# Kernel tuning notes

Hardware: AMD Instinct MI355X
Metric: run time of the kernel (lower is better)

The kernel has to match this reference:

```python
import jax, jax.numpy as jnp
from jax import lax
import numpy as np

H = 64  # hidden size

def lstm_layer(x, w_ih, w_hh, b_ih, b_hh):
    # x: [B,T,I]; w_ih: [4H,I]; w_hh: [4H,H]; gates ordered i,f,g,o (PyTorch)
    B = x.shape[0]
    xg = jnp.einsum('bti,gi->btg', x, w_ih) + b_ih  # precompute input projections [B,T,4H]
    h0 = jnp.zeros((B, H), x.dtype)
    c0 = jnp.zeros((B, H), x.dtype)
    def step(carry, xt):
        h, c = carry
        gates = xt + h @ w_hh.T + b_hh
        i, f, g, o = jnp.split(gates, 4, axis=-1)
        c = jax.nn.sigmoid(f) * c + jax.nn.sigmoid(i) * jnp.tanh(g)
        h = jax.nn.sigmoid(o) * jnp.tanh(c)
        return (h, c), h
    (hT, cT), hs = lax.scan(step, (h0, c0), jnp.swapaxes(xg, 0, 1))
    return jnp.swapaxes(hs, 0, 1), hT, cT

def layernorm(x, g, b, eps=1e-5):
    mu = jnp.mean(x, axis=-1, keepdims=True)
    var = jnp.mean(jnp.square(x - mu), axis=-1, keepdims=True)
    return (x - mu) * lax.rsqrt(var + eps) * g + b

def setup_inputs() -> dict:
    key = jax.random.key(0)
    ks = jax.random.split(key, 16)
    s = 0.05
    return {
        'x': jax.random.normal(ks[0], (512, 1024, 32), jnp.float32),
        'w_ih1': jax.random.normal(ks[1], (4 * H, 32)) * s,
        'w_hh1': jax.random.normal(ks[2], (4 * H, H)) * s,
        'b_ih1': jax.random.normal(ks[3], (4 * H,)) * s,
        'b_hh1': jax.random.normal(ks[4], (4 * H,)) * s,
        'w_ih2': jax.random.normal(ks[5], (4 * H, H)) * s,
        'w_hh2': jax.random.normal(ks[6], (4 * H, H)) * s,
        'b_ih2': jax.random.normal(ks[7], (4 * H,)) * s,
        'b_hh2': jax.random.normal(ks[8], (4 * H,)) * s,
        'fc1_w': jax.random.normal(ks[9], (128, H)) * s,
        'fc1_b': jax.random.normal(ks[10], (128,)) * s,
        'fc2_w': jax.random.normal(ks[11], (128, 128)) * s,
        'fc2_b': jax.random.normal(ks[12], (128,)) * s,
        'ln_g': jnp.ones((128,), jnp.float32),
        'ln_b': jnp.zeros((128,), jnp.float32),
    }

def reference(x, w_ih1, w_hh1, b_ih1, b_hh1, w_ih2, w_hh2, b_ih2, b_hh2,
              fc1_w, fc1_b, fc2_w, fc2_b, ln_g, ln_b):
    h1, _, _ = lstm_layer(x, w_ih1, w_hh1, b_ih1, b_hh1)
    # dropout(0.1) is identity in eval mode
    _, hT, _ = lstm_layer(h1, w_ih2, w_hh2, b_ih2, b_hh2)
    y = jax.nn.relu(hT @ fc1_w.T + fc1_b)
    y = y @ fc2_w.T + fc2_b
    return layernorm(y, ln_g, ln_b)
```

## Files before the change

### kernel.cpp

```cpp
#include <hip/hip_runtime.h>
#include <cstdint>
#include <cstddef>

#define T_STEPS 1024
#define NBLK    256
#define LOG2E   1.4426950408889634f

typedef __attribute__((ext_vector_type(8))) _Float16 half8;
typedef __attribute__((ext_vector_type(4))) _Float16 half4;
typedef __attribute__((ext_vector_type(4))) float    f32x4;
typedef __attribute__((ext_vector_type(4))) int      i32x4;

static __device__ __forceinline__ float fexp2(float x) {
#if defined(__has_builtin) && __has_builtin(__builtin_amdgcn_exp2f)
  return __builtin_amdgcn_exp2f(x);
#else
  return __exp2f(x);
#endif
}
static __device__ __forceinline__ float sigm2(float a) {
  return __builtin_amdgcn_rcpf(1.0f + fexp2(-a));
}
static __device__ __forceinline__ float tanhg2(float a) {
  return 2.0f * __builtin_amdgcn_rcpf(1.0f + fexp2(-(a + a))) - 1.0f;
}
static __device__ __forceinline__ float tanhc(float c) {
  return 1.0f - 2.0f * __builtin_amdgcn_rcpf(1.0f + fexp2(c * (2.0f * LOG2E)));
}

static __device__ __forceinline__ half8 load8s(const float* s, float sc) {
  float4 a = ((const float4*)s)[0];
  float4 b = ((const float4*)s)[1];
  half8 h;
  h[0] = (_Float16)(a.x * sc); h[1] = (_Float16)(a.y * sc);
  h[2] = (_Float16)(a.z * sc); h[3] = (_Float16)(a.w * sc);
  h[4] = (_Float16)(b.x * sc); h[5] = (_Float16)(b.y * sc);
  h[6] = (_Float16)(b.z * sc); h[7] = (_Float16)(b.w * sc);
  return h;
}
static __device__ __forceinline__ half4 cvt4(float4 v) {
  half4 h; h[0] = (_Float16)v.x; h[1] = (_Float16)v.y; h[2] = (_Float16)v.z; h[3] = (_Float16)v.w;
  return h;
}
static __device__ __forceinline__ i32x4 quant16(const float* src, float s) {
  union { i32x4 v; signed char b[16]; } u;
  #pragma unroll
  for (int j = 0; j < 16; ++j) u.b[j] = (signed char)__float2int_rn(src[j] * s);
  return u.v;
}

static __device__ __forceinline__ void barrier_lds() {
  __asm__ volatile("s_waitcnt lgkmcnt(0)\n\ts_barrier" ::: "memory");
}

__global__ __launch_bounds__(512, 2) void lstm_fused(
    const float* __restrict__ x,
    const float* __restrict__ w_ih1, const float* __restrict__ w_hh1,
    const float* __restrict__ b_ih1, const float* __restrict__ b_hh1,
    const float* __restrict__ w_ih2, const float* __restrict__ w_hh2,
    const float* __restrict__ b_ih2, const float* __restrict__ b_hh2,
    const float* __restrict__ fc1_w, const float* __restrict__ fc1_b,
    const float* __restrict__ fc2_w, const float* __restrict__ fc2_b,
    const float* __restrict__ ln_g, const float* __restrict__ ln_b,
    float* __restrict__ out)
{
  __shared__ __align__(16) signed char hs8[2][2][2][64];
  __shared__ __align__(16) _Float16 xbig[2][16][2][32];
  __shared__ __align__(16) float hfin[2][64];
  __shared__ __align__(16) float y1s[2][128];
  __shared__ __align__(16) float y2s[2][128];
  __shared__ float redmu[2], redrs[2];

  const int t   = threadIdx.x;
  const int b   = blockIdx.x;
  const int l   = t & 63;
  const int w   = t >> 6;
  const int ly  = w >> 2;
  const int wq  = w & 3;
  const int col = l & 15;
  const int q   = l >> 4;
  const int bm  = ((l & 15) >> 2) & 1;

  if (t < 512) ((signed char*)hs8)[t] = 0;

  if (t < 256) {
    const int b0 = t >> 7, r0 = t & 127, tr0 = r0 >> 3, ii0 = r0 & 7;
    const float4 v = *(const float4*)(x + ((size_t)(2 * b + b0) * T_STEPS + tr0) * 32 + ii0 * 4);
    *(half4*)((char*)xbig + tr0 * 128 + b0 * 64 + ii0 * 8) = cvt4(v);
  }

  half8 wbx[4];
  i32x4 wqa[4], wqb[4];
  float fs[4];
  {
    #pragma unroll
    for (int tt = 0; tt < 4; ++tt) {
      const int r = tt * 64 + wq * 16 + col;
      if (ly == 0) {
        wbx[tt] = load8s(w_ih1 + r * 32 + q * 8, LOG2E);
        const float* s1 = w_hh1 + r * 64 + q * 16;
        float m = 0.0f;
        #pragma unroll
        for (int j = 0; j < 16; ++j) m = fmaxf(m, fabsf(s1[j]));
        m = fmaxf(m, __shfl_xor(m, 16, 64));
        m = fmaxf(m, __shfl_xor(m, 32, 64));
        const float s = 127.0f / m;
        wqa[tt] = quant16(s1, s);
        wqb[tt] = wqa[tt];
        fs[tt] = m * (LOG2E / 16129.0f);
      } else {
        const float* s1 = w_ih2 + r * 64 + q * 16;
        const float* s2 = w_hh2 + r * 64 + q * 16;
        float m = 0.0f;
        #pragma unroll
        for (int j = 0; j < 16; ++j) m = fmaxf(m, fmaxf(fabsf(s1[j]), fabsf(s2[j])));
        m = fmaxf(m, __shfl_xor(m, 16, 64));
        m = fmaxf(m, __shfl_xor(m, 32, 64));
        const float s = 127.0f / m;
        wqa[tt] = quant16(s1, s);
        wqb[tt] = quant16(s2, s);
        fs[tt] = m * (LOG2E / 16129.0f);
      }
    }
  }

  float bia[4];
  f32x4 biav[4];
  {
    const float* bi_ = ly ? b_ih2 : b_ih1;
    const float* bh_ = ly ? b_hh2 : b_hh1;
    #pragma unroll
    for (int tt = 0; tt < 4; ++tt) {
      const int r = tt * 64 + wq * 16 + col;
      bia[tt] = (bi_[r] + bh_[r]) * LOG2E;
      biav[tt] = (f32x4){bia[tt], bia[tt], bia[tt], bia[tt]};
    }
  }
  const int u   = wq * 16 + col;
  const int abm = l >> 4;
  const int hwofs = ly * 128 + abm * 64 + u;

  const bool isx = (w < 4) && (l >= 32);
  const int g   = w * 32 + (l - 32);
  const int xtr = g >> 3;
  const int xii = g & 7;
  const float* xsrc0 = x + ((size_t)(2 * b + 0) * T_STEPS) * 32 + xii * 4;
  const float* xsrc1 = x + ((size_t)(2 * b + 1) * T_STEPS) * 32 + xii * 4;

  const char* h8base = (const char*)hs8  + bm * 64 + q * 16;
  const char* xwbase = (const char*)xbig + bm * 64 + q * 16;

  __syncthreads();

  half8 xf;
  i32x4 h1f;
  if (ly == 0) xf = *(const half8*)xwbase;

  float4 xv0 = make_float4(0.f, 0.f, 0.f, 0.f);
  float4 xv1 = make_float4(0.f, 0.f, 0.f, 0.f);
  float c = 0.0f;
  const i32x4 zi = (i32x4){0, 0, 0, 0};

  auto phase = [&](int p, int RD8, int WR8) {
    if (isx && (p & 15) == 0 && (p + 16 + xtr) < T_STEPS) {
      xv0 = *(const float4*)(xsrc0 + (size_t)(p + 16 + xtr) * 32);
      xv1 = *(const float4*)(xsrc1 + (size_t)(p + 16 + xtr) * 32);
    }

    if (ly == 0) {
      if (p < T_STEPS) {
        f32x4 accf[4];
        #pragma unroll
        for (int tt = 0; tt < 4; ++tt)
          accf[tt] = __builtin_amdgcn_mfma_f32_16x16x32_f16(xf, wbx[tt], biav[tt], 0, 0, 0);
        const i32x4 a1 = *(const i32x4*)(h8base + RD8);
        if (p + 1 < T_STEPS) {
          const int pn = p + 1;
          xf = *(const half8*)(xwbase + ((pn >> 4) & 1) * 2048 + (pn & 15) * 128);
        }
        i32x4 acci[4];
        #pragma unroll
        for (int tt = 0; tt < 4; ++tt)
          acci[tt] = __builtin_amdgcn_mfma_i32_16x16x64_i8(a1, wqa[tt], zi, 0, 0, 0);
        if (l < 32) {
          const float gi = sigm2 (accf[0][0] + fs[0] * (float)acci[0][0]);
          const float gf = sigm2 (accf[1][0] + fs[1] * (float)acci[1][0]);
          const float gg = tanhg2(accf[2][0] + fs[2] * (float)acci[2][0]);
          const float go = sigm2 (accf[3][0] + fs[3] * (float)acci[3][0]);
          c = gf * c + gi * gg;
          const float hv = go * tanhc(c);
          ((signed char*)hs8)[WR8 + hwofs] = (signed char)__float2int_rn(hv * 127.0f);
        }
      }
      if (isx && (p & 15) == 8 && (p + 8 + xtr) < T_STEPS) {
        const int bb2 = (((p >> 4) + 1) & 1) * 2048 + xtr * 128 + xii * 8;
        *(half4*)((char*)xbig + bb2)      = cvt4(xv0);
        *(half4*)((char*)xbig + bb2 + 64) = cvt4(xv1);
      }
    } else {
      i32x4 accq[4];
      if (p >= 2 && p <= T_STEPS + 1) {
        #pragma unroll
        for (int tt = 0; tt < 4; ++tt)
          accq[tt] = __builtin_amdgcn_mfma_i32_16x16x64_i8(h1f, wqa[tt], zi, 0, 0, 0);
      }
      i32x4 a2;
      if (p >= 2 && p <= T_STEPS + 1)
        a2 = *(const i32x4*)(h8base + RD8 + 128);
      if (p >= 1 && p <= T_STEPS)
        h1f = *(const i32x4*)(h8base + RD8);
      if (p >= 2 && p <= T_STEPS + 1) {
        i32x4 acci[4];
        #pragma unroll
        for (int tt = 0; tt < 4; ++tt)
          acci[tt] = __builtin_amdgcn_mfma_i32_16x16x64_i8(a2, wqb[tt], accq[tt], 0, 0, 0);
        if (l < 32) {
          const float gi = sigm2 (bia[0] + fs[0] * (float)acci[0][0]);
          const float gf = sigm2 (bia[1] + fs[1] * (float)acci[1][0]);
          const float gg = tanhg2(bia[2] + fs[2] * (float)acci[2][0]);
          const float go = sigm2 (bia[3] + fs[3] * (float)acci[3][0]);
          c = gf * c + gi * gg;
          const float hv = go * tanhc(c);
          ((signed char*)hs8)[WR8 + hwofs] = (signed char)__float2int_rn(hv * 127.0f);
          if (p == T_STEPS + 1) hfin[abm][u] = hv;
        }
      }
    }
  };

  for (int p2 = 0; p2 <= T_STEPS; p2 += 2) {
    phase(p2, 256, 0);
    barrier_lds();
    phase(p2 + 1, 0, 256);
    barrier_lds();
  }

  __syncthreads();

  if (t < 256) {
    const int bi = t >> 7, j = t & 127;
    float a = fc1_b[j];
    const float4* w4 = (const float4*)(fc1_w + j * 64);
    const float4* h4 = (const float4*)hfin[bi];
    #pragma unroll
    for (int qq = 0; qq < 16; ++qq) {
      float4 wv = w4[qq]; float4 hv = h4[qq];
      a += wv.x * hv.x + wv.y * hv.y + wv.z * hv.z + wv.w * hv.w;
    }
    y1s[bi][j] = fmaxf(a, 0.0f);
  }
  __syncthreads();
  if (t < 256) {
    const int bi = t >> 7, j = t & 127;
    float a = fc2_b[j];
    const float4* w4 = (const float4*)(fc2_w + j * 128);
    const float4* y4 = (const float4*)y1s[bi];
    #pragma unroll
    for (int qq = 0; qq < 32; ++qq) {
      float4 wv = w4[qq]; float4 yv = y4[qq];
      a += wv.x * yv.x + wv.y * yv.y + wv.z * yv.z + wv.w * yv.w;
    }
    y2s[bi][j] = a;
  }
  __syncthreads();
  if (t < 128) {
    const int bi = t >> 6, jj = t & 63;
    float s  = y2s[bi][jj] + y2s[bi][64 + jj];
    float qs = y2s[bi][jj] * y2s[bi][jj] + y2s[bi][64 + jj] * y2s[bi][64 + jj];
    #pragma unroll
    for (int off = 32; off > 0; off >>= 1) {
      s  += __shfl_down(s, off, 64);
      qs += __shfl_down(qs, off, 64);
    }
    if (jj == 0) {
      const float mu  = s * (1.0f / 128.0f);
      const float var = qs * (1.0f / 128.0f) - mu * mu;
      redmu[bi] = mu;
      redrs[bi] = rsqrtf(var + 1e-5f);
    }
  }
  __syncthreads();
  if (t < 256) {
    const int bi = t >> 7, j = t & 127;
    out[(size_t)(2 * b + bi) * 128 + j] =
        (y2s[bi][j] - redmu[bi]) * redrs[bi] * ln_g[j] + ln_b[j];
  }
}

extern "C" void kernel_launch(void* const* d_in, const int* in_sizes, int n_in,
                              void* d_out, int out_size, void* d_ws, size_t ws_size,
                              hipStream_t stream) {
  const float* x     = (const float*)d_in[0];
  const float* w_ih1 = (const float*)d_in[1];
  const float* w_hh1 = (const float*)d_in[2];
  const float* b_ih1 = (const float*)d_in[3];
  const float* b_hh1 = (const float*)d_in[4];
  const float* w_ih2 = (const float*)d_in[5];
  const float* w_hh2 = (const float*)d_in[6];
  const float* b_ih2 = (const float*)d_in[7];
  const float* b_hh2 = (const float*)d_in[8];
  const float* fc1_w = (const float*)d_in[9];
  const float* fc1_b = (const float*)d_in[10];
  const float* fc2_w = (const float*)d_in[11];
  const float* fc2_b = (const float*)d_in[12];
  const float* ln_g  = (const float*)d_in[13];
  const float* ln_b  = (const float*)d_in[14];
  float* out = (float*)d_out;

  lstm_fused<<<NBLK, 512, 0, stream>>>(x, w_ih1, w_hh1, b_ih1, b_hh1,
                                       w_ih2, w_hh2, b_ih2, b_hh2,
                                       fc1_w, fc1_b, fc2_w, fc2_b,
                                       ln_g, ln_b, out);
}
```

Before: 462.9 us.

## Restructure LSTM into warp-specialized segment pipeline with precomputed gate projections

```diff
diff --git a/kernel.cpp b/kernel.cpp
--- a/kernel.cpp
+++ b/kernel.cpp
@@ -3,11 +3,13 @@
 #include <cstddef>
 
 #define T_STEPS 1024
+#define SEG     8
+#define NSEG    (T_STEPS / SEG)
 #define NBLK    256
 #define LOG2E   1.4426950408889634f
+#define UPERM(k, c) ((((c) << 1) + ((k) & 1)) + (((k) >> 1) << 5))
 
 typedef __attribute__((ext_vector_type(8))) _Float16 half8;
-typedef __attribute__((ext_vector_type(4))) _Float16 half4;
 typedef __attribute__((ext_vector_type(4))) float    f32x4;
 typedef __attribute__((ext_vector_type(4))) int      i32x4;
 
@@ -38,10 +40,6 @@
   h[6] = (_Float16)(b.z * sc); h[7] = (_Float16)(b.w * sc);
   return h;
 }
-static __device__ __forceinline__ half4 cvt4(float4 v) {
-  half4 h; h[0] = (_Float16)v.x; h[1] = (_Float16)v.y; h[2] = (_Float16)v.z; h[3] = (_Float16)v.w;
-  return h;
-}
 static __device__ __forceinline__ i32x4 quant16(const float* src, float s) {
   union { i32x4 v; signed char b[16]; } u;
   #pragma unroll
@@ -53,7 +51,7 @@
   __asm__ volatile("s_waitcnt lgkmcnt(0)\n\ts_barrier" ::: "memory");
 }
 
-__global__ __launch_bounds__(512, 2) void lstm_fused(
+__global__ __launch_bounds__(256, 1) void lstm_fused(
     const float* __restrict__ x,
     const float* __restrict__ w_ih1, const float* __restrict__ w_hh1,
     const float* __restrict__ b_ih1, const float* __restrict__ b_hh1,
@@ -64,174 +62,214 @@
     const float* __restrict__ ln_g, const float* __restrict__ ln_b,
     float* __restrict__ out)
 {
-  __shared__ __align__(16) signed char hs8[2][2][2][64];
-  __shared__ __align__(16) _Float16 xbig[2][16][2][32];
+  __shared__ __align__(16) signed char h1ring[32][2][64];
+  __shared__ __align__(16) signed char h2ring[2][2][64];
+  __shared__ __align__(16) float xg1b[2][SEG][2][64][4];
+  __shared__ __align__(16) float xg2b[2][SEG][2][64][4];
   __shared__ __align__(16) float hfin[2][64];
   __shared__ __align__(16) float y1s[2][128];
   __shared__ __align__(16) float y2s[2][128];
   __shared__ float redmu[2], redrs[2];
 
   const int t   = threadIdx.x;
-  const int b   = blockIdx.x;
+  const int blk = blockIdx.x;
   const int l   = t & 63;
   const int w   = t >> 6;
-  const int ly  = w >> 2;
-  const int wq  = w & 3;
   const int col = l & 15;
   const int q   = l >> 4;
-  const int bm  = ((l & 15) >> 2) & 1;
-
-  if (t < 512) ((signed char*)hs8)[t] = 0;
-
-  if (t < 256) {
-    const int b0 = t >> 7, r0 = t & 127, tr0 = r0 >> 3, ii0 = r0 & 7;
-    const float4 v = *(const float4*)(x + ((size_t)(2 * b + b0) * T_STEPS + tr0) * 32 + ii0 * 4);
-    *(half4*)((char*)xbig + tr0 * 128 + b0 * 64 + ii0 * 8) = cvt4(v);
-  }
-
-  half8 wbx[4];
-  i32x4 wqa[4], wqb[4];
-  float fs[4];
+
   {
-    #pragma unroll
-    for (int tt = 0; tt < 4; ++tt) {
-      const int r = tt * 64 + wq * 16 + col;
-      if (ly == 0) {
-        wbx[tt] = load8s(w_ih1 + r * 32 + q * 8, LOG2E);
-        const float* s1 = w_hh1 + r * 64 + q * 16;
+    int* hp = (int*)h1ring;
+    #pragma unroll
+    for (int i = 0; i < 4; ++i) hp[t + i * 256] = 0;
+    if (t < 64) ((int*)h2ring)[t] = 0;
+  }
+
+  const i32x4 zi = (i32x4){0, 0, 0, 0};
+  f32x4 zf; zf[0] = 0.f; zf[1] = 0.f; zf[2] = 0.f; zf[3] = 0.f;
+
+  i32x4 wq[4][4];
+  half8 wbx[4][4];
+  f32x4 fsa0, fsa1;
+  float fsx[4][4];
+  float bL[4][4];
+
+  if (w < 3) {
+    const float* W = (w == 0) ? w_hh1 : (w == 1) ? w_hh2 : w_ih2;
+    float fs[4][4];
+    #pragma unroll
+    for (int g = 0; g < 4; ++g) {
+      #pragma unroll
+      for (int k = 0; k < 4; ++k) {
+        const int r = g * 64 + UPERM(k, col);
+        const float* p = W + r * 64 + q * 16;
         float m = 0.0f;
         #pragma unroll
-        for (int j = 0; j < 16; ++j) m = fmaxf(m, fabsf(s1[j]));
+        for (int j = 0; j < 16; ++j) m = fmaxf(m, fabsf(p[j]));
         m = fmaxf(m, __shfl_xor(m, 16, 64));
         m = fmaxf(m, __shfl_xor(m, 32, 64));
-        const float s = 127.0f / m;
-        wqa[tt] = quant16(s1, s);
-        wqb[tt] = wqa[tt];
-        fs[tt] = m * (LOG2E / 16129.0f);
-      } else {
-        const float* s1 = w_ih2 + r * 64 + q * 16;
-        const float* s2 = w_hh2 + r * 64 + q * 16;
-        float m = 0.0f;
+        wq[g][k] = quant16(p, 127.0f / m);
+        fs[g][k] = m * (LOG2E / 16129.0f);
+      }
+    }
+    if (w == 2) {
+      #pragma unroll
+      for (int g = 0; g < 4; ++g) {
         #pragma unroll
-        for (int j = 0; j < 16; ++j) m = fmaxf(m, fmaxf(fabsf(s1[j]), fabsf(s2[j])));
-        m = fmaxf(m, __shfl_xor(m, 16, 64));
-        m = fmaxf(m, __shfl_xor(m, 32, 64));
-        const float s = 127.0f / m;
-        wqa[tt] = quant16(s1, s);
-        wqb[tt] = quant16(s2, s);
-        fs[tt] = m * (LOG2E / 16129.0f);
-      }
-    }
-  }
-
-  float bia[4];
-  f32x4 biav[4];
-  {
-    const float* bi_ = ly ? b_ih2 : b_ih1;
-    const float* bh_ = ly ? b_hh2 : b_hh1;
-    #pragma unroll
-    for (int tt = 0; tt < 4; ++tt) {
-      const int r = tt * 64 + wq * 16 + col;
-      bia[tt] = (bi_[r] + bh_[r]) * LOG2E;
-      biav[tt] = (f32x4){bia[tt], bia[tt], bia[tt], bia[tt]};
-    }
-  }
-  const int u   = wq * 16 + col;
-  const int abm = l >> 4;
-  const int hwofs = ly * 128 + abm * 64 + u;
-
-  const bool isx = (w < 4) && (l >= 32);
-  const int g   = w * 32 + (l - 32);
-  const int xtr = g >> 3;
-  const int xii = g & 7;
-  const float* xsrc0 = x + ((size_t)(2 * b + 0) * T_STEPS) * 32 + xii * 4;
-  const float* xsrc1 = x + ((size_t)(2 * b + 1) * T_STEPS) * 32 + xii * 4;
-
-  const char* h8base = (const char*)hs8  + bm * 64 + q * 16;
-  const char* xwbase = (const char*)xbig + bm * 64 + q * 16;
-
-  __syncthreads();
-
-  half8 xf;
-  i32x4 h1f;
-  if (ly == 0) xf = *(const half8*)xwbase;
-
-  float4 xv0 = make_float4(0.f, 0.f, 0.f, 0.f);
-  float4 xv1 = make_float4(0.f, 0.f, 0.f, 0.f);
-  float c = 0.0f;
-  const i32x4 zi = (i32x4){0, 0, 0, 0};
-
-  auto phase = [&](int p, int RD8, int WR8) {
-    if (isx && (p & 15) == 0 && (p + 16 + xtr) < T_STEPS) {
-      xv0 = *(const float4*)(xsrc0 + (size_t)(p + 16 + xtr) * 32);
-      xv1 = *(const float4*)(xsrc1 + (size_t)(p + 16 + xtr) * 32);
-    }
-
-    if (ly == 0) {
-      if (p < T_STEPS) {
-        f32x4 accf[4];
+        for (int k = 0; k < 4; ++k) {
+          const int r = g * 64 + UPERM(k, col);
+          fsx[g][k] = fs[g][k];
+          bL[g][k]  = (b_ih2[r] + b_hh2[r]) * LOG2E;
+        }
+      }
+    } else if (l & 32) {
+      fsa0[0] = fs[0][2]; fsa0[1] = fs[1][2]; fsa0[2] = fs[2][2]; fsa0[3] = fs[3][2];
+      fsa1[0] = fs[0][3]; fsa1[1] = fs[1][3]; fsa1[2] = fs[2][3]; fsa1[3] = fs[3][3];
+    } else {
+      fsa0[0] = fs[0][0]; fsa0[1] = fs[1][0]; fsa0[2] = fs[2][0]; fsa0[3] = fs[3][0];
+      fsa1[0] = fs[0][1]; fsa1[1] = fs[1][1]; fsa1[2] = fs[2][1]; fsa1[3] = fs[3][1];
+    }
+  } else {
+    #pragma unroll
+    for (int g = 0; g < 4; ++g) {
+      #pragma unroll
+      for (int k = 0; k < 4; ++k) {
+        const int r = g * 64 + UPERM(k, col);
+        wbx[g][k] = load8s(w_ih1 + r * 32 + q * 8, LOG2E);
+        bL[g][k]  = (b_ih1[r] + b_hh1[r]) * LOG2E;
+      }
+    }
+  }
+
+  const int ab    = q & 1;
+  const int u0    = ((l & 15) << 1) + ((l >> 5) << 5);
+  const int bfrag = ((l & 15) >> 2) & 1;
+  const int hi    = l & 32;
+  const int arow  = (l & 15) >> 1;
+  const int axb   = l & 1;
+
+  float c0 = 0.0f, c1 = 0.0f;
+
+  auto produce_xg1 = [&](int tau) {
+    const float* xs = x + ((size_t)(2 * blk + axb) * T_STEPS + (tau * SEG + arow)) * 32 + q * 8;
+    const float4 va = ((const float4*)xs)[0];
+    const float4 vb = ((const float4*)xs)[1];
+    half8 xf;
+    xf[0] = (_Float16)va.x; xf[1] = (_Float16)va.y;
+    xf[2] = (_Float16)va.z; xf[3] = (_Float16)va.w;
+    xf[4] = (_Float16)vb.x; xf[5] = (_Float16)vb.y;
+    xf[6] = (_Float16)vb.z; xf[7] = (_Float16)vb.w;
+    f32x4 accf[4][4];
+    #pragma unroll
+    for (int g = 0; g < 4; ++g)
+      #pragma unroll
+      for (int k = 0; k < 4; ++k)
+        accf[g][k] = __builtin_amdgcn_mfma_f32_16x16x32_f16(xf, wbx[g][k], zf, 0, 0, 0);
+    float* dst = &xg1b[tau & 1][0][0][0][0];
+    #pragma unroll
+    for (int k = 0; k < 4; ++k) {
+      #pragma unroll
+      for (int r = 0; r < 4; ++r) {
+        const int row = q * 4 + r;
+        f32x4 v;
+        v[0] = accf[0][k][r] + bL[0][k];
+        v[1] = accf[1][k][r] + bL[1][k];
+        v[2] = accf[2][k][r] + bL[2][k];
+        v[3] = accf[3][k][r] + bL[3][k];
+        *(f32x4*)(dst + (size_t)(row * 64 + UPERM(k, col)) * 4) = v;
+      }
+    }
+  };
+
+  auto produce_xg2 = [&](int sg) {
+    const i32x4 a = *(const i32x4*)((const signed char*)h1ring +
+                    (size_t)((((sg * SEG + arow) & 31) * 128) + axb * 64 + q * 16));
+    i32x4 acc[4][4];
+    #pragma unroll
+    for (int g = 0; g < 4; ++g)
+      #pragma unroll
+      for (int k = 0; k < 4; ++k)
+        acc[g][k] = __builtin_amdgcn_mfma_i32_16x16x64_i8(a, wq[g][k], zi, 0, 0, 0);
+    float* dst = &xg2b[sg & 1][0][0][0][0];
+    #pragma unroll
+    for (int k = 0; k < 4; ++k) {
+      #pragma unroll
+      for (int r = 0; r < 4; ++r) {
+        const int row = q * 4 + r;
+        f32x4 v;
+        v[0] = bL[0][k] + fsx[0][k] * (float)acc[0][k][r];
+        v[1] = bL[1][k] + fsx[1][k] * (float)acc[1][k][r];
+        v[2] = bL[2][k] + fsx[2][k] * (float)acc[2][k][r];
+        v[3] = bL[3][k] + fsx[3][k] * (float)acc[3][k][r];
+        *(f32x4*)(dst + (size_t)(row * 64 + UPERM(k, col)) * 4) = v;
+      }
+    }
+  };
+
+  auto run_seg = [&](const float* XG, signed char* RING, int RM, int t0, int isl2) {
+    #pragma unroll
+    for (int j8 = 0; j8 < SEG; ++j8) {
+      const int tt = t0 + j8;
+      const i32x4 a = *(const i32x4*)(RING + ((tt - 1) & RM) * 128 + bfrag * 64 + q * 16);
+      const f32x4 xv0 = *(const f32x4*)(XG + (size_t)((j8 * 2 + ab) * 64 + u0) * 4);
+      const f32x4 xv1 = *(const f32x4*)(XG + (size_t)((j8 * 2 + ab) * 64 + u0 + 1) * 4);
+      i32x4 acc[4][4];
+      #pragma unroll
+      for (int g = 0; g < 4; ++g)
         #pragma unroll
-        for (int tt = 0; tt < 4; ++tt)
-          accf[tt] = __builtin_amdgcn_mfma_f32_16x16x32_f16(xf, wbx[tt], biav[tt], 0, 0, 0);
-        const i32x4 a1 = *(const i32x4*)(h8base + RD8);
-        if (p + 1 < T_STEPS) {
-          const int pn = p + 1;
-          xf = *(const half8*)(xwbase + ((pn >> 4) & 1) * 2048 + (pn & 15) * 128);
-        }
-        i32x4 acci[4];
-        #pragma unroll
-        for (int tt = 0; tt < 4; ++tt)
-          acci[tt] = __builtin_amdgcn_mfma_i32_16x16x64_i8(a1, wqa[tt], zi, 0, 0, 0);
-        if (l < 32) {
-          const float gi = sigm2 (accf[0][0] + fs[0] * (float)acci[0][0]);
-          const float gf = sigm2 (accf[1][0] + fs[1] * (float)acci[1][0]);
-          const float gg = tanhg2(accf[2][0] + fs[2] * (float)acci[2][0]);
-          const float go = sigm2 (accf[3][0] + fs[3] * (float)acci[3][0]);
-          c = gf * c + gi * gg;
-          const float hv = go * tanhc(c);
-          ((signed char*)hs8)[WR8 + hwofs] = (signed char)__float2int_rn(hv * 127.0f);
-        }
-      }
-      if (isx && (p & 15) == 8 && (p + 8 + xtr) < T_STEPS) {
-        const int bb2 = (((p >> 4) + 1) & 1) * 2048 + xtr * 128 + xii * 8;
-        *(half4*)((char*)xbig + bb2)      = cvt4(xv0);
-        *(half4*)((char*)xbig + bb2 + 64) = cvt4(xv1);
-      }
+        for (int k = 0; k < 4; ++k)
+          acc[g][k] = __builtin_amdgcn_mfma_i32_16x16x64_i8(a, wq[g][k], zi, 0, 0, 0);
+      const int i00 = hi ? acc[0][2][0] : acc[0][0][0];
+      const int i01 = hi ? acc[1][2][0] : acc[1][0][0];
+      const int i02 = hi ? acc[2][2][0] : acc[2][0][0];
+      const int i03 = hi ? acc[3][2][0] : acc[3][0][0];
+      const float p00 = xv0[0] + fsa0[0] * (float)i00;
+      const float p01 = xv0[1] + fsa0[1] * (float)i01;
+      const float p02 = xv0[2] + fsa0[2] * (float)i02;
+      const float p03 = xv0[3] + fsa0[3] * (float)i03;
+      const float gi0 = sigm2(p00), gf0 = sigm2(p01);
+      const float gg0 = tanhg2(p02), go0 = sigm2(p03);
+      c0 = gf0 * c0 + gi0 * gg0;
+      const float h0 = go0 * tanhc(c0);
+      const int i10 = hi ? acc[0][3][0] : acc[0][1][0];
+      const int i11 = hi ? acc[1][3][0] : acc[1][1][0];
+      const int i12 = hi ? acc[2][3][0] : acc[2][1][0];
+      const int i13 = hi ? acc[3][3][0] : acc[3][1][0];
+      const float p10 = xv1[0] + fsa1[0] * (float)i10;
+      const float p11 = xv1[1] + fsa1[1] * (float)i11;
+      const float p12 = xv1[2] + fsa1[2] * (float)i12;
+      const float p13 = xv1[3] + fsa1[3] * (float)i13;
+      const float gi1 = sigm2(p10), gf1 = sigm2(p11);
+      const float gg1 = tanhg2(p12), go1 = sigm2(p13);
+      c1 = gf1 * c1 + gi1 * gg1;
+      const float h1v = go1 * tanhc(c1);
+      signed char* wp = RING + (tt & RM) * 128 + ab * 64 + u0;
+      wp[0] = (signed char)__float2int_rn(h0  * 127.0f);
+      wp[1] = (signed char)__float2int_rn(h1v * 127.0f);
+      if (isl2 && tt == T_STEPS - 1) {
+        hfin[ab][u0]     = h0;
+        hfin[ab][u0 + 1] = h1v;
+      }
+    }
+  };
+
+  if (w == 3) produce_xg1(0);
+  barrier_lds();
+
+  for (int s = 0; s <= NSEG + 1; ++s) {
+    if (w == 0) {
+      if (s < NSEG)
+        run_seg(&xg1b[s & 1][0][0][0][0], (signed char*)h1ring, 31, s * SEG, 0);
+    } else if (w == 1) {
+      const int sg = s - 2;
+      if (sg >= 0)
+        run_seg(&xg2b[sg & 1][0][0][0][0], (signed char*)h2ring, 1, sg * SEG, 1);
+    } else if (w == 2) {
+      const int sg = s - 1;
+      if (sg >= 0 && sg < NSEG) produce_xg2(sg);
     } else {
-      i32x4 accq[4];
-      if (p >= 2 && p <= T_STEPS + 1) {
-        #pragma unroll
-        for (int tt = 0; tt < 4; ++tt)
-          accq[tt] = __builtin_amdgcn_mfma_i32_16x16x64_i8(h1f, wqa[tt], zi, 0, 0, 0);
-      }
-      i32x4 a2;
-      if (p >= 2 && p <= T_STEPS + 1)
-        a2 = *(const i32x4*)(h8base + RD8 + 128);
-      if (p >= 1 && p <= T_STEPS)
-        h1f = *(const i32x4*)(h8base + RD8);
-      if (p >= 2 && p <= T_STEPS + 1) {
-        i32x4 acci[4];
-        #pragma unroll
-        for (int tt = 0; tt < 4; ++tt)
-          acci[tt] = __builtin_amdgcn_mfma_i32_16x16x64_i8(a2, wqb[tt], accq[tt], 0, 0, 0);
-        if (l < 32) {
-          const float gi = sigm2 (bia[0] + fs[0] * (float)acci[0][0]);
-          const float gf = sigm2 (bia[1] + fs[1] * (float)acci[1][0]);
-          const float gg = tanhg2(bia[2] + fs[2] * (float)acci[2][0]);
-          const float go = sigm2 (bia[3] + fs[3] * (float)acci[3][0]);
-          c = gf * c + gi * gg;
-          const float hv = go * tanhc(c);
-          ((signed char*)hs8)[WR8 + hwofs] = (signed char)__float2int_rn(hv * 127.0f);
-          if (p == T_STEPS + 1) hfin[abm][u] = hv;
-        }
-      }
-    }
-  };
-
-  for (int p2 = 0; p2 <= T_STEPS; p2 += 2) {
-    phase(p2, 256, 0);
-    barrier_lds();
-    phase(p2 + 1, 0, 256);
+      if (s + 1 < NSEG) produce_xg1(s + 1);
+    }
     barrier_lds();
   }
 
@@ -239,28 +277,28 @@
 
   if (t < 256) {
     const int bi = t >> 7, j = t & 127;
-    float a = fc1_b[j];
+    float accv = fc1_b[j];
     const float4* w4 = (const float4*)(fc1_w + j * 64);
     const float4* h4 = (const float4*)hfin[bi];
     #pragma unroll
     for (int qq = 0; qq < 16; ++qq) {
       float4 wv = w4[qq]; float4 hv = h4[qq];
-      a += wv.x * hv.x + wv.y * hv.y + wv.z * hv.z + wv.w * hv.w;
-    }
-    y1s[bi][j] = fmaxf(a, 0.0f);
+      accv += wv.x * hv.x + wv.y * hv.y + wv.z * hv.z + wv.w * hv.w;
+    }
+    y1s[bi][j] = fmaxf(accv, 0.0f);
   }
   __syncthreads();
   if (t < 256) {
     const int bi = t >> 7, j = t & 127;
-    float a = fc2_b[j];
+    float accv = fc2_b[j];
     const float4* w4 = (const float4*)(fc2_w + j * 128);
     const float4* y4 = (const float4*)y1s[bi];
     #pragma unroll
     for (int qq = 0; qq < 32; ++qq) {
       float4 wv = w4[qq]; float4 yv = y4[qq];
-      a += wv.x * yv.x + wv.y * yv.y + wv.z * yv.z + wv.w * yv.w;
-    }
-    y2s[bi][j] = a;
+      accv += wv.x * yv.x + wv.y * yv.y + wv.z * yv.z + wv.w * yv.w;
+    }
+    y2s[bi][j] = accv;
   }
   __syncthreads();
   if (t < 128) {
@@ -282,7 +320,7 @@
   __syncthreads();
   if (t < 256) {
     const int bi = t >> 7, j = t & 127;
-    out[(size_t)(2 * b + bi) * 128 + j] =
+    out[(size_t)(2 * blk + bi) * 128 + j] =
         (y2s[bi][j] - redmu[bi]) * redrs[bi] * ln_g[j] + ln_b[j];
   }
 }
@@ -307,7 +345,7 @@
   const float* ln_b  = (const float*)d_in[14];
   float* out = (float*)d_out;
 
-  lstm_fused<<<NBLK, 512, 0, stream>>>(x, w_ih1, w_hh1, b_ih1, b_hh1,
+  lstm_fused<<<NBLK, 256, 0, stream>>>(x, w_ih1, w_hh1, b_ih1, b_hh1,
                                        w_ih2, w_hh2, b_ih2, b_hh2,
                                        fc1_w, fc1_b, fc2_w, fc2_b,
                                        ln_g, ln_b, out);
```

Result: slower. 480.2 us (+3.7%).
